# Kernel tuning notes

Hardware: AMD Instinct MI355X
Metric: run time of the kernel (lower is better)

The kernel has to match this reference:

```python
import jax, jax.numpy as jnp
import numpy as np

D_MODEL = 1024
N_HEADS = 16
NUM_KV_HEADS = 4
D_K = D_MODEL // N_HEADS
ROPE_BASE = 10000.0


def apply_rotary_emb(x, base=ROPE_BASE):
    # x: [B, H, T, D], half-split rotation over positions 0..T-1
    B, H, T, D = x.shape
    inv_freq = 1.0 / (base ** (jnp.arange(0, D, 2, dtype=jnp.float32) / D))  # [D/2]
    ang = jnp.arange(T, dtype=jnp.float32)[:, None] * inv_freq[None, :]      # [T, D/2]
    cos = jnp.cos(ang)[None, None].astype(x.dtype)
    sin = jnp.sin(ang)[None, None].astype(x.dtype)
    x1, x2 = x[..., : D // 2], x[..., D // 2 :]
    return jnp.concatenate([x1 * cos - x2 * sin, x2 * cos + x1 * sin], axis=-1)


def setup_inputs() -> dict:
    key = jax.random.key(0)
    ks = jax.random.split(key, 6)
    B, Tq, Tkv = 4, 2048, 2048
    query = jax.random.normal(ks[0], (B, Tq, D_MODEL), dtype=jnp.float32)
    key_value = jax.random.normal(ks[1], (B, Tkv, D_MODEL), dtype=jnp.float32)
    query_mask = jnp.ones((B, Tq), dtype=jnp.bool_)
    kv_mask = jnp.ones((B, Tkv), dtype=jnp.bool_)
    s = 0.02
    w_q = jax.random.normal(ks[2], (D_MODEL, D_MODEL), dtype=jnp.float32) * s
    w_k = jax.random.normal(ks[3], (NUM_KV_HEADS * D_K, D_MODEL), dtype=jnp.float32) * s
    w_v = jax.random.normal(ks[4], (NUM_KV_HEADS * D_K, D_MODEL), dtype=jnp.float32) * s
    w_out = jax.random.normal(ks[5], (D_MODEL, D_MODEL), dtype=jnp.float32) * s
    return {"query": query, "key_value": key_value, "query_mask": query_mask,
            "kv_mask": kv_mask, "w_q": w_q, "w_k": w_k, "w_v": w_v, "w_out": w_out}


def reference(query, key_value, query_mask, kv_mask, w_q, w_k, w_v, w_out):
    B, Tq, _ = query.shape
    Tkv = key_value.shape[1]
    group = N_HEADS // NUM_KV_HEADS
    # projections (torch Linear: x @ W.T)
    Q = (query @ w_q.T).reshape(B, Tq, N_HEADS, D_K).transpose(0, 2, 1, 3)        # [B,H,Tq,D]
    K = (key_value @ w_k.T).reshape(B, Tkv, NUM_KV_HEADS, D_K).transpose(0, 2, 1, 3)
    V = (key_value @ w_v.T).reshape(B, Tkv, NUM_KV_HEADS, D_K).transpose(0, 2, 1, 3)
    # RoPE on Q and K
    Q = apply_rotary_emb(Q)
    K = apply_rotary_emb(K)
    # GQA: repeat kv heads
    K = jnp.repeat(K, group, axis=1)  # [B,H,Tkv,D]
    V = jnp.repeat(V, group, axis=1)
    # mask: [B,1,Tq,Tkv]
    attn_mask = (kv_mask[:, None, None, :] & query_mask[:, None, :, None])
    scale = 1.0 / jnp.sqrt(jnp.asarray(D_K, dtype=Q.dtype))
    scores = jnp.einsum("bhqd,bhkd->bhqk", Q, K) * scale
    scores = jnp.where(attn_mask, scores, jnp.asarray(-jnp.inf, dtype=scores.dtype))
    attn = jax.nn.softmax(scores, axis=-1)
    out = jnp.einsum("bhqk,bhkd->bhqd", attn, V)
    out = out.transpose(0, 2, 1, 3).reshape(B, Tq, D_MODEL)
    out = out @ w_out.T
    return out
```

## Files before the change

### kernel.cpp

```cpp
#include <hip/hip_runtime.h>
#include <hip/hip_bf16.h>
#include <hip/hip_fp16.h>

#define B_    4
#define TQ    2048
#define TKV   2048
#define DM    1024
#define NH    16
#define NKV   4
#define DK    64

typedef _Float16 f16x8 __attribute__((ext_vector_type(8)));
typedef _Float16 f16x4 __attribute__((ext_vector_type(4)));
typedef float    f32x4 __attribute__((ext_vector_type(4)));
typedef float    f32x16 __attribute__((ext_vector_type(16)));

__device__ __forceinline__ void store1(float* p, float v) { *p = v; }
__device__ __forceinline__ void store1(__half* p, float v) {
  union { __half h; unsigned short u; } c; c.h = __float2half(v);
  *(unsigned short*)p = c.u;
}

__device__ __forceinline__ f16x4 load4h(const float* p) {
  float4 v = *(const float4*)p;
  f16x4 r;
  r[0] = (_Float16)v.x; r[1] = (_Float16)v.y;
  r[2] = (_Float16)v.z; r[3] = (_Float16)v.w;
  return r;
}
__device__ __forceinline__ f16x4 load4h(const __half* p) {
  return *(const f16x4*)p;
}

__device__ __forceinline__ unsigned pack2h(float a, float b) {
  auto pk = __builtin_amdgcn_cvt_pkrtz(a, b);
  unsigned u;
  __builtin_memcpy(&u, &pk, 4);
  return u;
}

__global__ void zero_out_kernel(float* out, int n) {
  int i = blockIdx.x * blockDim.x + threadIdx.x;
  if (i < n) out[i] = 0.0f;
}

#define GAP 40
#define BM 64
#define BN 128
template <typename AT, typename CT>
__global__ __launch_bounds__(256) void gemm_proj(
    const AT* __restrict__ A0, const AT* __restrict__ A1,
    const float* __restrict__ W0, const float* __restrict__ W1,
    const float* __restrict__ W2,
    CT* __restrict__ C0, CT* __restrict__ C1, CT* __restrict__ C2,
    int N0, int Nkv, int K) {
  const int bid = blockIdx.x;
  const AT* __restrict__ A;
  const float* __restrict__ W;
  CT* __restrict__ C;
  int N, bx, by;
  if (bid < 1024) {
    A = A0; W = W0; C = C0; N = N0;
    bx = bid & 7; by = bid >> 3;
  } else {
    int r = bid - 1024;
    A = A1; N = Nkv;
    if (r < 256) { W = W1; C = C1; } else { W = W2; C = C2; r -= 256; }
    bx = r & 1; by = r >> 1;
  }

  __shared__ _Float16 As[2 * BM * GAP];
  __shared__ _Float16 Ws[2 * BN * GAP];

  const int t = threadIdx.x;
  const int w = t >> 6, l = t & 63;
  const int lm = l & 15, quad = l >> 4;
  const int wm = (w >> 1) * 32, wn = (w & 1) * 64;
  const int m0 = by * BM, n0 = bx * BN;

  const int srow = t >> 3;
  const int scol = (t & 7) * 4;

  f32x4 acc[2][4] = {};
  f16x4 av[2], wv[4];
#pragma unroll
  for (int p = 0; p < 2; ++p)
    av[p] = load4h(&A[(size_t)(m0 + srow + p * 32) * K + scol]);
#pragma unroll
  for (int p = 0; p < 4; ++p)
    wv[p] = load4h(&W[(size_t)(n0 + srow + p * 32) * K + scol]);

  int cur = 0;
  for (int k0 = 0; k0 < K; k0 += 32) {
    _Float16* as = &As[cur * BM * GAP];
    _Float16* ws = &Ws[cur * BN * GAP];
#pragma unroll
    for (int p = 0; p < 2; ++p)
      *(f16x4*)&as[(srow + p * 32) * GAP + scol] = av[p];
#pragma unroll
    for (int p = 0; p < 4; ++p)
      *(f16x4*)&ws[(srow + p * 32) * GAP + scol] = wv[p];
    __syncthreads();
    if (k0 + 32 < K) {
#pragma unroll
      for (int p = 0; p < 2; ++p)
        av[p] = load4h(&A[(size_t)(m0 + srow + p * 32) * K + k0 + 32 + scol]);
#pragma unroll
      for (int p = 0; p < 4; ++p)
        wv[p] = load4h(&W[(size_t)(n0 + srow + p * 32) * K + k0 + 32 + scol]);
    }

    f16x8 af[2], bf[4];
#pragma unroll
    for (int i = 0; i < 2; ++i)
      af[i] = *(const f16x8*)&as[(wm + i * 16 + lm) * GAP + quad * 8];
#pragma unroll
    for (int j = 0; j < 4; ++j)
      bf[j] = *(const f16x8*)&ws[(wn + j * 16 + lm) * GAP + quad * 8];
#pragma unroll
    for (int i = 0; i < 2; ++i)
#pragma unroll
      for (int j = 0; j < 4; ++j)
        acc[i][j] =
            __builtin_amdgcn_mfma_f32_16x16x32_f16(af[i], bf[j], acc[i][j], 0, 0, 0);
    cur ^= 1;
  }

#pragma unroll
  for (int i = 0; i < 2; ++i)
#pragma unroll
    for (int r = 0; r < 4; ++r) {
      size_t row = (size_t)(m0 + wm + i * 16 + quad * 4 + r) * N;
#pragma unroll
      for (int j = 0; j < 4; ++j)
        store1(&C[row + n0 + wn + j * 16 + lm], acc[i][j][r]);
    }
}

__global__ void rope_kernel(__half* __restrict__ X, int T, int H, int total_pairs) {
  int idx = blockIdx.x * blockDim.x + threadIdx.x;
  if (idx >= total_pairs) return;
  int i   = idx & 31;
  int h   = (idx >> 5) % H;
  int row = idx / (32 * H);
  int tpos = row % T;
  __half* p = X + ((size_t)row * H + h) * DK;
  float inv = exp2f((float)i * -0.41524101186091403f);
  float ang = (float)tpos * inv;
  float c, s;
  sincosf(ang, &s, &c);
  float x1 = __half2float(p[i]), x2 = __half2float(p[i + 32]);
  p[i]      = __float2half(x1 * c - x2 * s);
  p[i + 32] = __float2half(x2 * c + x1 * s);
}

#define AP 72
#define C2 0.18033688011112042f
#define RLOG2 -0.41524101186091403f
__global__ __launch_bounds__(256, 3) void attn_mfma(const __half* Q,
                                                    const __half* __restrict__ K,
                                                    const __half* __restrict__ V,
                                                    __half* O) {
  __shared__ _Float16 Ks[64 * AP];
  __shared__ _Float16 Vt[64 * AP];
  const int t = threadIdx.x;
  const int w = t >> 6, l = t & 63;
  const int lq = l & 31, hi = l >> 5;
  const int qt = blockIdx.x, h = blockIdx.y, b = blockIdx.z;
  const int kvh = h >> 2;

  const __half* qbase =
      Q + (((size_t)b * TQ + qt * 128 + w * 32 + lq) * NH + h) * DK;
  f16x8 aq[4];
#pragma unroll
  for (int kc = 0; kc < 4; ++kc)
    aq[kc] = *(const f16x8*)(qbase + kc * 16 + hi * 8);

  {
    const float tpos = (float)(qt * 128 + w * 32 + lq);
#pragma unroll
    for (int kc = 0; kc < 2; ++kc)
#pragma unroll
      for (int j = 0; j < 8; ++j) {
        int d = kc * 16 + hi * 8 + j;
        float inv = exp2f((float)d * RLOG2);
        float ang = tpos * inv;
        float c, s;
        sincosf(ang, &s, &c);
        float x1 = (float)aq[kc][j], x2 = (float)aq[kc + 2][j];
        aq[kc][j]     = (_Float16)((x1 * c - x2 * s) * C2);
        aq[kc + 2][j] = (_Float16)((x2 * c + x1 * s) * C2);
      }
  }

  const int skey = t >> 3, sdseg = t & 7;
  const int vkey = t & 63, vdb0 = (t >> 6) * 8;
  const __half* kp0 =
      K + (((size_t)b * TKV + skey) * NKV + kvh) * DK + sdseg * 8;
  const __half* kp1 = kp0 + (size_t)32 * NKV * DK;
  const __half* vp0 =
      V + (((size_t)b * TKV + vkey) * NKV + kvh) * DK + vdb0;
  const __half* vp1 = vp0 + 32;
  const size_t kstep = (size_t)64 * NKV * DK;

  f16x8 kpre0 = *(const f16x8*)kp0, kpre1 = *(const f16x8*)kp1;
  f16x8 vpre0 = *(const f16x8*)vp0, vpre1 = *(const f16x8*)vp1;

  f32x16 o_acc[2];
#pragma unroll
  for (int i = 0; i < 16; ++i) { o_acc[0][i] = 0.f; o_acc[1][i] = 0.f; }
  float m_run = -1e30f, l_run = 0.0f;

  for (int ck = 0; ck < TKV / 64; ++ck) {
    __syncthreads();
    *(f16x8*)&Ks[skey * AP + sdseg * 8] = kpre0;
    *(f16x8*)&Ks[(skey + 32) * AP + sdseg * 8] = kpre1;
#pragma unroll
    for (int j = 0; j < 8; ++j) {
      Vt[(vdb0 + j) * AP + vkey] = vpre0[j];
      Vt[(vdb0 + 32 + j) * AP + vkey] = vpre1[j];
    }
    __syncthreads();
    if (ck + 1 < TKV / 64) {
      size_t off = (size_t)(ck + 1) * kstep;
      kpre0 = *(const f16x8*)(kp0 + off);
      kpre1 = *(const f16x8*)(kp1 + off);
      vpre0 = *(const f16x8*)(vp0 + off);
      vpre1 = *(const f16x8*)(vp1 + off);
    }

#pragma unroll
    for (int tile = 0; tile < 2; ++tile) {
      f32x16 st;
#pragma unroll
      for (int i = 0; i < 16; ++i) st[i] = 0.f;
      __builtin_amdgcn_s_setprio(1);
#pragma unroll
      for (int kc = 0; kc < 4; ++kc) {
        f16x8 ak =
            *(const f16x8*)&Ks[(tile * 32 + lq) * AP + kc * 16 + hi * 8];
        st = __builtin_amdgcn_mfma_f32_32x32x16_f16(ak, aq[kc], st, 0, 0, 0);
      }
      __builtin_amdgcn_s_setprio(0);

      float vmax = st[0];
#pragma unroll
      for (int i = 1; i < 16; ++i) vmax = fmaxf(vmax, st[i]);
      vmax = fmaxf(vmax, __shfl_xor(vmax, 32));

      if (!__all(vmax - m_run <= 8.0f)) {
        float m_new = fmaxf(m_run, vmax);
        float alpha = exp2f(m_run - m_new);
        m_run = m_new;
        l_run *= alpha;
#pragma unroll
        for (int reg = 0; reg < 16; ++reg) {
          int row = (reg & 3) + 8 * (reg >> 2) + 4 * hi;
          float ar = __shfl(alpha, row);
          o_acc[0][reg] *= ar;
          o_acc[1][reg] *= ar;
        }
      }

      unsigned q16u[8];
      float psum = 0.0f;
#pragma unroll
      for (int rr = 0; rr < 8; ++rr) {
        float p0 = exp2f(st[2 * rr] - m_run);
        float p1 = exp2f(st[2 * rr + 1] - m_run);
        psum += p0 + p1;
        q16u[rr] = pack2h(p0, p1);
      }
      psum += __shfl_xor(psum, 32);
      l_run += psum;

      __builtin_amdgcn_s_setprio(1);
#pragma unroll
      for (int kb = 0; kb < 2; ++kb) {
        const int base = kb * 4;
        union { unsigned u[4]; f16x8 v; } ap;
#pragma unroll
        for (int c = 0; c < 2; ++c) {
          unsigned R0 = q16u[base + c];
          unsigned R1 = q16u[base + 2 + c];
          unsigned Z = hi ? R0 : R1;
          unsigned Xp = __shfl_xor(Z, 32);
          ap.u[c]     = hi ? Xp : R0;
          ap.u[c + 2] = hi ? R1 : Xp;
        }
#pragma unroll
        for (int nt = 0; nt < 2; ++nt) {
          f16x8 bv = *(const f16x8*)&Vt[(nt * 32 + lq) * AP + tile * 32 +
                                        kb * 16 + hi * 8];
          o_acc[nt] =
              __builtin_amdgcn_mfma_f32_32x32x16_f16(ap.v, bv, o_acc[nt], 0, 0, 0);
        }
      }
      __builtin_amdgcn_s_setprio(0);
    }
  }

#pragma unroll
  for (int reg = 0; reg < 16; ++reg) {
    int row = (reg & 3) + 8 * (reg >> 2) + 4 * hi;
    float inv = 1.0f / __shfl(l_run, row);
    size_t orow =
        (((size_t)b * TQ + qt * 128 + w * 32 + row) * NH + h) * DK;
    O[orow + lq]      = __float2half(o_acc[0][reg] * inv);
    O[orow + 32 + lq] = __float2half(o_acc[1][reg] * inv);
  }
}

extern "C" void kernel_launch(void* const* d_in, const int* in_sizes, int n_in,
                              void* d_out, int out_size, void* d_ws, size_t ws_size,
                              hipStream_t stream) {
  int iq, ikv, iwq, iwk, iwv, iwo;
  bool ok = true;
  if (n_in >= 8 && in_sizes[0] == 8388608 && in_sizes[1] == 8388608) {
    iq = 0; ikv = 1; iwq = 4; iwk = 5; iwv = 6; iwo = 7;
  } else if (n_in >= 8 && in_sizes[0] == 8388608 && in_sizes[1] == 8192) {
    ikv = 0; iq = 2; iwk = 4; iwo = 5; iwq = 6; iwv = 7;
  } else if (n_in == 6 && in_sizes[2] == 1048576) {
    iq = 0; ikv = 1; iwq = 2; iwk = 3; iwv = 4; iwo = 5;
  } else if (n_in == 6 && in_sizes[2] == 262144) {
    ikv = 0; iq = 1; iwk = 2; iwo = 3; iwq = 4; iwv = 5;
  } else {
    ok = false; iq = ikv = iwq = iwk = iwv = iwo = 0;
  }

  const size_t nQ  = (size_t)B_ * TQ * DM;
  const size_t nKV = (size_t)B_ * TKV * NKV * DK;
  const size_t need = (nQ + 2 * nKV) * sizeof(__half);
  if (!ok || ws_size < need) {
    zero_out_kernel<<<(out_size + 255) / 256, 256, 0, stream>>>((float*)d_out,
                                                                out_size);
    return;
  }

  const float* query     = (const float*)d_in[iq];
  const float* key_value = (const float*)d_in[ikv];
  const float* w_q   = (const float*)d_in[iwq];
  const float* w_k   = (const float*)d_in[iwk];
  const float* w_v   = (const float*)d_in[iwv];
  const float* w_out = (const float*)d_in[iwo];
  float* out = (float*)d_out;

  __half* Qh = (__half*)d_ws;
  __half* Kh = Qh + nQ;
  __half* Vh = Kh + nKV;

  dim3 blk(256);
  gemm_proj<<<dim3(1536), blk, 0, stream>>>(query, key_value, w_q, w_k, w_v,
                                            Qh, Kh, Vh, DM, NKV * DK, DM);
  int pk = B_ * TKV * NKV * 32;
  rope_kernel<<<(pk + 255) / 256, blk, 0, stream>>>(Kh, TKV, NKV, pk);
  attn_mfma<<<dim3(TQ / 128, NH, B_), dim3(256), 0, stream>>>(Qh, Kh, Vh, Qh);
  gemm_proj<<<dim3(1024), blk, 0, stream>>>(Qh, Qh, w_out, w_out, w_out,
                                            out, out, out, DM, DM, DM);
}
```

Baseline: 363.8 us.

## Process full 64-key chunk per softmax step and compute row sums via MFMA

The attention loop now computes scores for both 32-key tiles before running one online-softmax update per 64-key chunk, which halves the max/rescale passes. The row sum is accumulated with an extra MFMA against a ones vector instead of a VALU sum plus shuffle. The softmax scale moves from the Q preload into the exponent, and occupancy is lowered from 3 to 2 blocks per CU to make room for the added registers. The weight-load conversion also switches to packed cvt_pkrtz. These changes trade extra MFMA work and lower occupancy for less VALU and shuffle work.

```diff
diff --git a/kernel.cpp b/kernel.cpp
--- a/kernel.cpp
+++ b/kernel.cpp
@@ -21,22 +21,22 @@
   *(unsigned short*)p = c.u;
 }
 
-__device__ __forceinline__ f16x4 load4h(const float* p) {
-  float4 v = *(const float4*)p;
-  f16x4 r;
-  r[0] = (_Float16)v.x; r[1] = (_Float16)v.y;
-  r[2] = (_Float16)v.z; r[3] = (_Float16)v.w;
-  return r;
-}
-__device__ __forceinline__ f16x4 load4h(const __half* p) {
-  return *(const f16x4*)p;
-}
-
 __device__ __forceinline__ unsigned pack2h(float a, float b) {
   auto pk = __builtin_amdgcn_cvt_pkrtz(a, b);
   unsigned u;
   __builtin_memcpy(&u, &pk, 4);
   return u;
+}
+
+__device__ __forceinline__ f16x4 load4h(const float* p) {
+  float4 v = *(const float4*)p;
+  union { unsigned u[2]; f16x4 h; } c;
+  c.u[0] = pack2h(v.x, v.y);
+  c.u[1] = pack2h(v.z, v.w);
+  return c.h;
+}
+__device__ __forceinline__ f16x4 load4h(const __half* p) {
+  return *(const f16x4*)p;
 }
 
 __global__ void zero_out_kernel(float* out, int n) {
@@ -157,7 +157,7 @@
 #define AP 72
 #define C2 0.18033688011112042f
 #define RLOG2 -0.41524101186091403f
-__global__ __launch_bounds__(256, 3) void attn_mfma(const __half* Q,
+__global__ __launch_bounds__(256, 2) void attn_mfma(const __half* Q,
                                                     const __half* __restrict__ K,
                                                     const __half* __restrict__ V,
                                                     __half* O) {
@@ -188,10 +188,12 @@
         float c, s;
         sincosf(ang, &s, &c);
         float x1 = (float)aq[kc][j], x2 = (float)aq[kc + 2][j];
-        aq[kc][j]     = (_Float16)((x1 * c - x2 * s) * C2);
-        aq[kc + 2][j] = (_Float16)((x2 * c + x1 * s) * C2);
-      }
-  }
+        aq[kc][j]     = (_Float16)(x1 * c - x2 * s);
+        aq[kc + 2][j] = (_Float16)(x2 * c + x1 * s);
+      }
+  }
+
+  const f16x8 vones = {1.f16, 1.f16, 1.f16, 1.f16, 1.f16, 1.f16, 1.f16, 1.f16};
 
   const int skey = t >> 3, sdseg = t & 7;
   const int vkey = t & 63, vdb0 = (t >> 6) * 8;
@@ -206,10 +208,10 @@
   f16x8 kpre0 = *(const f16x8*)kp0, kpre1 = *(const f16x8*)kp1;
   f16x8 vpre0 = *(const f16x8*)vp0, vpre1 = *(const f16x8*)vp1;
 
-  f32x16 o_acc[2];
-#pragma unroll
-  for (int i = 0; i < 16; ++i) { o_acc[0][i] = 0.f; o_acc[1][i] = 0.f; }
-  float m_run = -1e30f, l_run = 0.0f;
+  f32x16 o_acc[2], l_acc;
+#pragma unroll
+  for (int i = 0; i < 16; ++i) { o_acc[0][i] = 0.f; o_acc[1][i] = 0.f; l_acc[i] = 0.f; }
+  float m_run = -1e30f;
 
   for (int ck = 0; ck < TKV / 64; ++ck) {
     __syncthreads();
@@ -229,81 +231,82 @@
       vpre1 = *(const f16x8*)(vp1 + off);
     }
 
-#pragma unroll
-    for (int tile = 0; tile < 2; ++tile) {
-      f32x16 st;
-#pragma unroll
-      for (int i = 0; i < 16; ++i) st[i] = 0.f;
-      __builtin_amdgcn_s_setprio(1);
+    f32x16 st[2];
+#pragma unroll
+    for (int i = 0; i < 16; ++i) { st[0][i] = 0.f; st[1][i] = 0.f; }
+    __builtin_amdgcn_s_setprio(1);
+#pragma unroll
+    for (int tile = 0; tile < 2; ++tile)
 #pragma unroll
       for (int kc = 0; kc < 4; ++kc) {
         f16x8 ak =
             *(const f16x8*)&Ks[(tile * 32 + lq) * AP + kc * 16 + hi * 8];
-        st = __builtin_amdgcn_mfma_f32_32x32x16_f16(ak, aq[kc], st, 0, 0, 0);
-      }
-      __builtin_amdgcn_s_setprio(0);
-
-      float vmax = st[0];
-#pragma unroll
-      for (int i = 1; i < 16; ++i) vmax = fmaxf(vmax, st[i]);
-      vmax = fmaxf(vmax, __shfl_xor(vmax, 32));
-
-      if (!__all(vmax - m_run <= 8.0f)) {
-        float m_new = fmaxf(m_run, vmax);
-        float alpha = exp2f(m_run - m_new);
-        m_run = m_new;
-        l_run *= alpha;
-#pragma unroll
-        for (int reg = 0; reg < 16; ++reg) {
-          int row = (reg & 3) + 8 * (reg >> 2) + 4 * hi;
-          float ar = __shfl(alpha, row);
-          o_acc[0][reg] *= ar;
-          o_acc[1][reg] *= ar;
-        }
-      }
-
-      unsigned q16u[8];
-      float psum = 0.0f;
+        st[tile] =
+            __builtin_amdgcn_mfma_f32_32x32x16_f16(ak, aq[kc], st[tile], 0, 0, 0);
+      }
+    __builtin_amdgcn_s_setprio(0);
+
+    float vmax = st[0][0];
+#pragma unroll
+    for (int i = 1; i < 16; ++i) vmax = fmaxf(vmax, st[0][i]);
+#pragma unroll
+    for (int i = 0; i < 16; ++i) vmax = fmaxf(vmax, st[1][i]);
+    vmax *= C2;
+    vmax = fmaxf(vmax, __shfl_xor(vmax, 32));
+
+    if (!__all(vmax - m_run <= 8.0f)) {
+      float m_new = fmaxf(m_run, vmax);
+      float alpha = exp2f(m_run - m_new);
+      m_run = m_new;
+#pragma unroll
+      for (int reg = 0; reg < 16; ++reg) {
+        int row = (reg & 3) + 8 * (reg >> 2) + 4 * hi;
+        float ar = __shfl(alpha, row);
+        l_acc[reg] *= ar;
+        o_acc[0][reg] *= ar;
+        o_acc[1][reg] *= ar;
+      }
+    }
+
+    unsigned q16u[2][8];
+#pragma unroll
+    for (int tile = 0; tile < 2; ++tile)
 #pragma unroll
       for (int rr = 0; rr < 8; ++rr) {
-        float p0 = exp2f(st[2 * rr] - m_run);
-        float p1 = exp2f(st[2 * rr + 1] - m_run);
-        psum += p0 + p1;
-        q16u[rr] = pack2h(p0, p1);
-      }
-      psum += __shfl_xor(psum, 32);
-      l_run += psum;
-
-      __builtin_amdgcn_s_setprio(1);
-#pragma unroll
-      for (int kb = 0; kb < 2; ++kb) {
-        const int base = kb * 4;
-        union { unsigned u[4]; f16x8 v; } ap;
-#pragma unroll
-        for (int c = 0; c < 2; ++c) {
-          unsigned R0 = q16u[base + c];
-          unsigned R1 = q16u[base + 2 + c];
-          unsigned Z = hi ? R0 : R1;
-          unsigned Xp = __shfl_xor(Z, 32);
-          ap.u[c]     = hi ? Xp : R0;
-          ap.u[c + 2] = hi ? R1 : Xp;
-        }
-#pragma unroll
-        for (int nt = 0; nt < 2; ++nt) {
-          f16x8 bv = *(const f16x8*)&Vt[(nt * 32 + lq) * AP + tile * 32 +
-                                        kb * 16 + hi * 8];
-          o_acc[nt] =
-              __builtin_amdgcn_mfma_f32_32x32x16_f16(ap.v, bv, o_acc[nt], 0, 0, 0);
-        }
-      }
-      __builtin_amdgcn_s_setprio(0);
-    }
+        float p0 = exp2f(st[tile][2 * rr] * C2 - m_run);
+        float p1 = exp2f(st[tile][2 * rr + 1] * C2 - m_run);
+        q16u[tile][rr] = pack2h(p0, p1);
+      }
+
+    __builtin_amdgcn_s_setprio(1);
+#pragma unroll
+    for (int kb = 0; kb < 4; ++kb) {
+      const int tl = kb >> 1, base = (kb & 1) * 4;
+      union { unsigned u[4]; f16x8 v; } ap;
+#pragma unroll
+      for (int c = 0; c < 2; ++c) {
+        unsigned R0 = q16u[tl][base + c];
+        unsigned R1 = q16u[tl][base + 2 + c];
+        unsigned Z = hi ? R0 : R1;
+        unsigned Xp = __shfl_xor(Z, 32);
+        ap.u[c]     = hi ? Xp : R0;
+        ap.u[c + 2] = hi ? R1 : Xp;
+      }
+      l_acc = __builtin_amdgcn_mfma_f32_32x32x16_f16(ap.v, vones, l_acc, 0, 0, 0);
+#pragma unroll
+      for (int nt = 0; nt < 2; ++nt) {
+        f16x8 bv = *(const f16x8*)&Vt[(nt * 32 + lq) * AP + kb * 16 + hi * 8];
+        o_acc[nt] =
+            __builtin_amdgcn_mfma_f32_32x32x16_f16(ap.v, bv, o_acc[nt], 0, 0, 0);
+      }
+    }
+    __builtin_amdgcn_s_setprio(0);
   }
 
 #pragma unroll
   for (int reg = 0; reg < 16; ++reg) {
     int row = (reg & 3) + 8 * (reg >> 2) + 4 * hi;
-    float inv = 1.0f / __shfl(l_run, row);
+    float inv = 1.0f / l_acc[reg];
     size_t orow =
         (((size_t)b * TQ + qt * 128 + w * 32 + row) * NH + h) * DK;
     O[orow + lq]      = __float2half(o_acc[0][reg] * inv);
```

Result: no change. 359.4 us (-1.2%).
